# Optimization experiments

Hardware: AMD Instinct MI355X
Metric: run time of the kernel (lower is better)

Reference implementation:

```python
import jax, jax.numpy as jnp
import numpy as np

N_NODES = 65536
N_EDGES = 524288
IN_CH = 128
FHC = 256      # first_hc = max(hidden, in)
HID = 256
NCLS = 3
NODES_PER_GRAPH = 32


def setup_inputs() -> dict:
    key = jax.random.key(0)
    ks = jax.random.split(key, 16)
    s = 1.0 / np.sqrt(FHC)
    inp = {
        "x": jax.random.normal(ks[0], (N_NODES, IN_CH), dtype=jnp.float32),
        "edge_index": jax.random.randint(ks[1], (2, N_EDGES), 0, N_NODES, dtype=jnp.int64),
        "edge_attr": jax.random.uniform(ks[2], (N_EDGES,), dtype=jnp.float32),
        # GatedGraphConv params: per-layer matmul weight + GRUCell
        "gg_w": jax.random.uniform(ks[3], (2, FHC, FHC), minval=-s, maxval=s, dtype=jnp.float32),
        "w_ih": jax.random.uniform(ks[4], (3 * FHC, FHC), minval=-s, maxval=s, dtype=jnp.float32),
        "w_hh": jax.random.uniform(ks[5], (3 * FHC, FHC), minval=-s, maxval=s, dtype=jnp.float32),
        "b_ih": jax.random.uniform(ks[6], (3 * FHC,), minval=-s, maxval=s, dtype=jnp.float32),
        "b_hh": jax.random.uniform(ks[7], (3 * FHC,), minval=-s, maxval=s, dtype=jnp.float32),
        # Conv1d(FHC, 1, kernel_size=1)
        "cnn_w": jax.random.uniform(ks[8], (1, FHC, 1), minval=-s, maxval=s, dtype=jnp.float32),
        "cnn_b": jax.random.uniform(ks[9], (1,), minval=-s, maxval=s, dtype=jnp.float32),
        # Linear(32, HID), Linear(HID, NCLS)
        "lin1_w": jax.random.uniform(ks[10], (HID, NODES_PER_GRAPH), minval=-0.17, maxval=0.17, dtype=jnp.float32),
        "lin1_b": jax.random.uniform(ks[11], (HID,), minval=-0.17, maxval=0.17, dtype=jnp.float32),
        "lin2_w": jax.random.uniform(ks[12], (NCLS, HID), minval=-s, maxval=s, dtype=jnp.float32),
        "lin2_b": jax.random.uniform(ks[13], (NCLS,), minval=-s, maxval=s, dtype=jnp.float32),
    }
    return inp


def _gated_graph_conv(x, src, dst, edge_w, gg_w, w_ih, w_hh, b_ih, b_hh):
    # PyG GatedGraphConv: pad input to out_channels, then num_layers iterations.
    n = x.shape[0]
    h = jnp.pad(x, ((0, 0), (0, FHC - x.shape[1])))  # [N, FHC]
    for i in range(2):
        m = h @ gg_w[i]                                   # [N, FHC]
        msgs = m[src] * edge_w[:, None]                   # gather per edge [E, FHC]
        agg = jax.ops.segment_sum(msgs, dst, num_segments=n)  # scatter-add [N, FHC]
        # GRUCell(input=agg, hidden=h), torch gate order: r, z, n
        gi = agg @ w_ih.T + b_ih
        gh = h @ w_hh.T + b_hh
        ir, iz, ig = jnp.split(gi, 3, axis=1)
        hr, hz, hg = jnp.split(gh, 3, axis=1)
        r = jax.nn.sigmoid(ir + hr)
        z = jax.nn.sigmoid(iz + hz)
        g = jnp.tanh(ig + r * hg)
        h = (1.0 - z) * g + z * h
    return h


def reference(x, edge_index, edge_attr, gg_w, w_ih, w_hh, b_ih, b_hh,
              cnn_w, cnn_b, lin1_w, lin1_b, lin2_w, lin2_b):
    src, dst = edge_index[0], edge_index[1]
    h = _gated_graph_conv(x, src, dst, edge_attr, gg_w, w_ih, w_hh, b_ih, b_hh)
    h = jax.nn.relu(h)  # dropout is identity in eval mode
    bs = h.shape[0] // NODES_PER_GRAPH
    h = h.reshape(bs, NODES_PER_GRAPH, FHC)          # (bs e) f -> bs e f
    # Conv1d(FHC,1,k=1) over layout (bs, f, e): y[b,e] = sum_f w[0,f,0]*h[b,e,f] + b
    y = jnp.einsum('bef,f->be', h, cnn_w[:, :, 0].reshape(FHC)) + cnn_b[0]
    y = jax.nn.relu(y)                               # [bs, 32]
    y = y @ lin1_w.T + lin1_b
    y = jax.nn.relu(y)
    y = y @ lin2_w.T + lin2_b
    return jax.nn.softmax(y, axis=-1)
```

## Files before the change

kernel.cpp:

```cpp
#include <hip/hip_runtime.h>
#include <math.h>

#define N_NODES 65536
#define N_EDGES 524288
#define IN_CH 128
#define FHC 256
#define NCLS 3
#define NPG 32
#define NGRAPH (N_NODES / NPG)

typedef __attribute__((ext_vector_type(8))) short bfrag;
typedef __attribute__((ext_vector_type(4))) float facc;

__device__ inline float sigmoidf_(float x) { return 1.0f / (1.0f + expf(-x)); }

__device__ __forceinline__ float fast_sigmoid(float x) {
    return __builtin_amdgcn_rcpf(1.0f + __expf(-x));
}
__device__ __forceinline__ float fast_tanh(float x) {
    return 1.0f - 2.0f * __builtin_amdgcn_rcpf(__expf(2.0f * x) + 1.0f);
}

__device__ inline short f2bf(float f) {
    union { float f; unsigned u; } v; v.f = f;
    unsigned r = v.u + 0x7fffu + ((v.u >> 16) & 1u);
    return (short)(r >> 16);
}
__device__ inline float bf2f(short s) {
    union { unsigned u; float f; } v; v.u = ((unsigned)(unsigned short)s) << 16;
    return v.f;
}

__device__ __forceinline__ void gld16(const short* g, short* l) {
    __builtin_amdgcn_global_load_lds(
        (const __attribute__((address_space(1))) void*)g,
        (__attribute__((address_space(3))) void*)l, 16, 0, 0);
}

__global__ void convert_kernel(const float* __restrict__ gg_w, const float* __restrict__ wih,
                               const float* __restrict__ whh, short* __restrict__ ggT,
                               short* __restrict__ wih16, short* __restrict__ whh16) {
    int t = blockIdx.x * 256 + threadIdx.x;
    if (t < 2 * FHC * FHC) {
        int i = t >> 16, r = t & 65535, n = r >> 8, k = r & 255;
        ggT[t] = f2bf(gg_w[i * FHC * FHC + k * FHC + n]);
    } else if (t < 2 * FHC * FHC + 3 * FHC * FHC) {
        int u = t - 2 * FHC * FHC;
        wih16[u] = f2bf(wih[u]);
    } else {
        int u = t - 5 * FHC * FHC;
        whh16[u] = f2bf(whh[u]);
    }
}

__global__ void pad16_kernel(const float* __restrict__ x, short* __restrict__ h) {
    int idx = blockIdx.x * 256 + threadIdx.x;
    int c4 = idx & 63, n = idx >> 6;
    short4 v = {0, 0, 0, 0};
    if (c4 < 32) {
        float4 xv = reinterpret_cast<const float4*>(x)[n * 32 + c4];
        v.x = f2bf(xv.x); v.y = f2bf(xv.y); v.z = f2bf(xv.z); v.w = f2bf(xv.w);
    }
    reinterpret_cast<short4*>(h)[idx] = v;
}

__global__ void hist_kernel(const int* __restrict__ ei, int* __restrict__ deg) {
    int e = blockIdx.x * 256 + threadIdx.x;
    atomicAdd(&deg[ei[N_EDGES + e]], 1);
}

__global__ void scan_reduce_kernel(const int* __restrict__ deg, int* __restrict__ bsum) {
    __shared__ int s[256];
    int t = threadIdx.x;
    s[t] = deg[blockIdx.x * 256 + t];
    __syncthreads();
    for (int off = 128; off > 0; off >>= 1) {
        if (t < off) s[t] += s[t + off];
        __syncthreads();
    }
    if (t == 0) bsum[blockIdx.x] = s[0];
}

__global__ void scan_bsum_kernel(const int* __restrict__ bsum, int* __restrict__ boff) {
    __shared__ int s[256];
    int t = threadIdx.x;
    int v = bsum[t];
    s[t] = v;
    __syncthreads();
    for (int off = 1; off < 256; off <<= 1) {
        int u = (t >= off) ? s[t - off] : 0;
        __syncthreads();
        s[t] += u;
        __syncthreads();
    }
    boff[t] = s[t] - v;
}

__global__ void scan_write_kernel(const int* __restrict__ deg, const int* __restrict__ boff,
                                  int* __restrict__ rowptr, int* __restrict__ cur) {
    __shared__ int s[256];
    int t = threadIdx.x, gid = blockIdx.x * 256 + t;
    int v = deg[gid];
    s[t] = v;
    __syncthreads();
    for (int off = 1; off < 256; off <<= 1) {
        int u = (t >= off) ? s[t - off] : 0;
        __syncthreads();
        s[t] += u;
        __syncthreads();
    }
    int excl = boff[blockIdx.x] + s[t] - v;
    rowptr[gid] = excl;
    cur[gid] = excl;
    if (gid == N_NODES - 1) rowptr[N_NODES] = excl + v;
}

__global__ void fill_kernel(const int* __restrict__ ei, const float* __restrict__ ea,
                            int* __restrict__ cur, int2* __restrict__ csr) {
    int e = blockIdx.x * 256 + threadIdx.x;
    int dst = ei[N_EDGES + e];
    int pos = atomicAdd(&cur[dst], 1);
    csr[pos] = make_int2(ei[e], __float_as_int(ea[e]));
}

__global__ __launch_bounds__(256) void gather_kernel(const short* __restrict__ m,
                                                     const int* __restrict__ rowptr,
                                                     const int2* __restrict__ csr,
                                                     short* __restrict__ agg16) {
    int node = blockIdx.x * 4 + (threadIdx.x >> 6);
    int lane = threadIdx.x & 63;
    int beg = rowptr[node], end = rowptr[node + 1];
    const short4* m4 = reinterpret_cast<const short4*>(m);
    float a0 = 0.f, a1 = 0.f, a2 = 0.f, a3 = 0.f;
#define GSTEP(E)                                            \
    {                                                       \
        float w = __int_as_float((E).y);                    \
        short4 v = m4[(size_t)(E).x * 64 + lane];           \
        a0 += bf2f(v.x) * w;                                \
        a1 += bf2f(v.y) * w;                                \
        a2 += bf2f(v.z) * w;                                \
        a3 += bf2f(v.w) * w;                                \
    }
    int j = beg;
    for (; j + 8 <= end; j += 8) {
        int2 e0 = csr[j + 0], e1 = csr[j + 1], e2 = csr[j + 2], e3 = csr[j + 3];
        int2 e4 = csr[j + 4], e5 = csr[j + 5], e6 = csr[j + 6], e7 = csr[j + 7];
        GSTEP(e0) GSTEP(e1) GSTEP(e2) GSTEP(e3)
        GSTEP(e4) GSTEP(e5) GSTEP(e6) GSTEP(e7)
    }
    for (; j + 2 <= end; j += 2) {
        int2 e0 = csr[j + 0], e1 = csr[j + 1];
        GSTEP(e0) GSTEP(e1)
    }
    if (j < end) {
        int2 e0 = csr[j];
        GSTEP(e0)
    }
#undef GSTEP
    short4 o;
    o.x = f2bf(a0); o.y = f2bf(a1); o.z = f2bf(a2); o.w = f2bf(a3);
    reinterpret_cast<short4*>(agg16)[(size_t)node * 64 + lane] = o;
}

__global__ __launch_bounds__(256, 2) void mgemm_kernel(const short* __restrict__ A,
                                                       const short* __restrict__ W,
                                                       short* __restrict__ C) {
    __shared__ __align__(16) short As[128 * 32];
    __shared__ __align__(16) short Ws[128 * 32];
    int tid = threadIdx.x;
    int lane = tid & 63, wv = tid >> 6, fr = lane & 15, fc = lane >> 4;
    int m0 = blockIdx.x * 128, n0 = blockIdx.y * 128;
    int srow = lane >> 2;
    int scol = (lane & 3) ^ ((lane >> 3) & 3);
    const short* gsrc[4];
    short* ldst[4];
#pragma unroll
    for (int i = 0; i < 4; ++i) {
        int ch = wv * 4 + i;
        if (ch < 8) {
            ldst[i] = &As[ch * 512];
            gsrc[i] = A + (size_t)(m0 + ch * 16 + srow) * FHC + scol * 8;
        } else {
            ldst[i] = &Ws[(ch - 8) * 512];
            gsrc[i] = W + (size_t)(n0 + (ch - 8) * 16 + srow) * FHC + scol * 8;
        }
    }
    int fcs = fc ^ ((fr >> 1) & 3);
    facc acc[2][8] = {};
    for (int k0 = 0; k0 < FHC; k0 += 32) {
#pragma unroll
        for (int i = 0; i < 4; ++i) gld16(gsrc[i] + k0, ldst[i]);
        __syncthreads();
        int ar = (wv * 32 + fr) * 32 + fcs * 8;
        bfrag a0 = *reinterpret_cast<bfrag*>(&As[ar]);
        bfrag a1 = *reinterpret_cast<bfrag*>(&As[ar + 16 * 32]);
#pragma unroll
        for (int cf = 0; cf < 8; ++cf) {
            bfrag b = *reinterpret_cast<bfrag*>(&Ws[(cf * 16 + fr) * 32 + fcs * 8]);
            acc[0][cf] = __builtin_amdgcn_mfma_f32_16x16x32_bf16(a0, b, acc[0][cf], 0, 0, 0);
            acc[1][cf] = __builtin_amdgcn_mfma_f32_16x16x32_bf16(a1, b, acc[1][cf], 0, 0, 0);
        }
        __syncthreads();
    }
#pragma unroll
    for (int s = 0; s < 2; ++s)
#pragma unroll
        for (int cf = 0; cf < 8; ++cf)
#pragma unroll
            for (int r = 0; r < 4; ++r) {
                int node = m0 + wv * 32 + s * 16 + fc * 4 + r;
                int c = n0 + cf * 16 + fr;
                C[(size_t)node * FHC + c] = f2bf(acc[s][cf][r]);
            }
}

__global__ __launch_bounds__(256, 2) void gru_mfma_kernel(
    const short* __restrict__ agg16, const short* __restrict__ hin, short* __restrict__ hout,
    const short* __restrict__ wih16, const short* __restrict__ whh16,
    const float* __restrict__ bih, const float* __restrict__ bhh) {
    __shared__ __align__(16) short lds[2 * 16 * 512];
    int tid = threadIdx.x;
    int lane = tid & 63, wv = tid >> 6, fr = lane & 15, fc = lane >> 4;
    int c = blockIdx.y * 64 + wv * 16 + fr;

    bfrag wreg[6][8];
    {
        size_t roff = (size_t)c * FHC + fc * 8;
#pragma unroll
        for (int ks = 0; ks < 8; ++ks) {
            wreg[0][ks] = *reinterpret_cast<const bfrag*>(wih16 + roff + ks * 32);
            wreg[1][ks] = *reinterpret_cast<const bfrag*>(wih16 + (size_t)256 * FHC + roff + ks * 32);
            wreg[2][ks] = *reinterpret_cast<const bfrag*>(wih16 + (size_t)512 * FHC + roff + ks * 32);
            wreg[3][ks] = *reinterpret_cast<const bfrag*>(whh16 + roff + ks * 32);
            wreg[4][ks] = *reinterpret_cast<const bfrag*>(whh16 + (size_t)256 * FHC + roff + ks * 32);
            wreg[5][ks] = *reinterpret_cast<const bfrag*>(whh16 + (size_t)512 * FHC + roff + ks * 32);
        }
    }
    float br = bih[c] + bhh[c];
    float bz = bih[c + 256] + bhh[c + 256];
    float big = bih[c + 512], bhg = bhh[c + 512];

    int srow = lane >> 2;
    int scol = (lane & 3) ^ ((lane >> 3) & 3);
    const short* gb[4];
    int ldsoff[4];
#pragma unroll
    for (int i = 0; i < 4; ++i) {
        int ch = wv * 4 + i;
        int mat = ch >> 3, ks = ch & 7;
        const short* src = mat ? hin : agg16;
        gb[i] = src + (size_t)srow * FHC + ks * 32 + scol * 8;
        ldsoff[i] = ch * 512;
    }
    int fcs = fc ^ ((fr >> 1) & 3);
    int lo = (fr * 4 + fcs) * 8;
    const int NT = 32;
    int tile0 = blockIdx.x * NT;

    int hbase = (8 + (c >> 5)) * 512 + (c & 7);
    int hg = (c >> 3) & 3;

    auto STAGE = [&](int t, int bufsel) {
        size_t noff = (size_t)(tile0 + t) * 16 * FHC;
        short* dst = &lds[bufsel * 8192];
#pragma unroll
        for (int i = 0; i < 4; ++i) gld16(gb[i] + noff, dst + ldsoff[i]);
    };

    STAGE(0, 0);
    for (int t = 0; t < NT; ++t) {
        int cur = t & 1;
        if (t + 1 < NT) {
            STAGE(t + 1, cur ^ 1);
            asm volatile("s_waitcnt vmcnt(8)" ::: "memory");
        } else {
            asm volatile("s_waitcnt vmcnt(0)" ::: "memory");
        }
        __builtin_amdgcn_sched_barrier(0);
        __builtin_amdgcn_s_barrier();
        const short* B = &lds[cur * 8192];
        facc aR = {}, aZ = {}, aG = {}, aH = {};
#pragma unroll
        for (int ks = 0; ks < 8; ++ks) {
            bfrag ag = *reinterpret_cast<const bfrag*>(B + ks * 512 + lo);
            bfrag hh = *reinterpret_cast<const bfrag*>(B + (8 + ks) * 512 + lo);
            aR = __builtin_amdgcn_mfma_f32_16x16x32_bf16(ag, wreg[0][ks], aR, 0, 0, 0);
            aR = __builtin_amdgcn_mfma_f32_16x16x32_bf16(hh, wreg[3][ks], aR, 0, 0, 0);
            aZ = __builtin_amdgcn_mfma_f32_16x16x32_bf16(ag, wreg[1][ks], aZ, 0, 0, 0);
            aZ = __builtin_amdgcn_mfma_f32_16x16x32_bf16(hh, wreg[4][ks], aZ, 0, 0, 0);
            aG = __builtin_amdgcn_mfma_f32_16x16x32_bf16(ag, wreg[2][ks], aG, 0, 0, 0);
            aH = __builtin_amdgcn_mfma_f32_16x16x32_bf16(hh, wreg[5][ks], aH, 0, 0, 0);
        }
        int node0 = (tile0 + t) * 16;
#pragma unroll
        for (int r = 0; r < 4; ++r) {
            int row = fc * 4 + r;
            float hold = bf2f(B[hbase + (row * 4 + (hg ^ ((row >> 1) & 3))) * 8]);
            float rg = fast_sigmoid(aR[r] + br);
            float z = fast_sigmoid(aZ[r] + bz);
            float g = fast_tanh(aG[r] + big + rg * (aH[r] + bhg));
            hout[(size_t)(node0 + row) * FHC + c] = f2bf(g + z * (hold - g));
        }
        __builtin_amdgcn_s_barrier();
    }
}

__global__ void cnn_kernel(const short* __restrict__ h, const float* __restrict__ w,
                           const float* __restrict__ b, float* __restrict__ y1) {
    int node = blockIdx.x * 4 + (threadIdx.x >> 6);
    int lane = threadIdx.x & 63;
    short4 hv = reinterpret_cast<const short4*>(h)[(size_t)node * 64 + lane];
    float4 wv = reinterpret_cast<const float4*>(w)[lane];
    float p = fmaxf(bf2f(hv.x), 0.f) * wv.x + fmaxf(bf2f(hv.y), 0.f) * wv.y +
              fmaxf(bf2f(hv.z), 0.f) * wv.z + fmaxf(bf2f(hv.w), 0.f) * wv.w;
#pragma unroll
    for (int off = 32; off > 0; off >>= 1) p += __shfl_down(p, off, 64);
    if (lane == 0) y1[node] = fmaxf(p + b[0], 0.f);
}

__global__ __launch_bounds__(256) void head_kernel(
    const float* __restrict__ y1, const float* __restrict__ l1w,
    const float* __restrict__ l1b, const float* __restrict__ l2w,
    const float* __restrict__ l2b, float* __restrict__ out) {
    __shared__ float ys[32];
    __shared__ float zs[256];
    __shared__ float os[3];
    int b = blockIdx.x, tid = threadIdx.x;
    if (tid < 32) ys[tid] = y1[b * 32 + tid];
    __syncthreads();
    float acc = l1b[tid];
#pragma unroll
    for (int k = 0; k < 32; ++k) acc += ys[k] * l1w[tid * 32 + k];
    zs[tid] = fmaxf(acc, 0.f);
    __syncthreads();
    int wave = tid >> 6, lane = tid & 63;
    if (wave < 3) {
        float p = 0.f;
#pragma unroll
        for (int j = 0; j < 4; ++j) p += zs[lane + j * 64] * l2w[wave * 256 + lane + j * 64];
#pragma unroll
        for (int off = 32; off > 0; off >>= 1) p += __shfl_down(p, off, 64);
        if (lane == 0) os[wave] = p + l2b[wave];
    }
    __syncthreads();
    if (tid == 0) {
        float mx = fmaxf(os[0], fmaxf(os[1], os[2]));
        float e0 = expf(os[0] - mx), e1 = expf(os[1] - mx), e2 = expf(os[2] - mx);
        float s = e0 + e1 + e2;
        out[b * 3 + 0] = e0 / s;
        out[b * 3 + 1] = e1 / s;
        out[b * 3 + 2] = e2 / s;
    }
}

extern "C" void kernel_launch(void* const* d_in, const int* in_sizes, int n_in,
                              void* d_out, int out_size, void* d_ws, size_t ws_size,
                              hipStream_t stream) {
    const float* x = (const float*)d_in[0];
    const int* ei = (const int*)d_in[1];
    const float* ea = (const float*)d_in[2];
    const float* gg_w = (const float*)d_in[3];
    const float* w_ih = (const float*)d_in[4];
    const float* w_hh = (const float*)d_in[5];
    const float* b_ih = (const float*)d_in[6];
    const float* b_hh = (const float*)d_in[7];
    const float* cnn_w = (const float*)d_in[8];
    const float* cnn_b = (const float*)d_in[9];
    const float* l1w = (const float*)d_in[10];
    const float* l1b = (const float*)d_in[11];
    const float* l2w = (const float*)d_in[12];
    const float* l2b = (const float*)d_in[13];
    float* out = (float*)d_out;

    const size_t nodeE = (size_t)N_NODES * FHC;
    char* p = (char*)d_ws;
    short* hA = (short*)p;      p += nodeE * 2;
    short* hB = (short*)p;      p += nodeE * 2;
    short* m16 = (short*)p;     p += nodeE * 2;
    short* agg16 = (short*)p;   p += nodeE * 2;
    short* ggT = (short*)p;     p += (size_t)2 * FHC * FHC * 2;
    short* wih16 = (short*)p;   p += (size_t)3 * FHC * FHC * 2;
    short* whh16 = (short*)p;   p += (size_t)3 * FHC * FHC * 2;
    float* y1 = (float*)p;      p += (size_t)N_NODES * 4;
    int* deg = (int*)p;         p += (size_t)N_NODES * 4;
    int* rowptr = (int*)p;      p += (size_t)(N_NODES + 4) * 4;
    int* cur = (int*)p;         p += (size_t)N_NODES * 4;
    int* bsum = (int*)p;        p += 256 * 4;
    int* boff = (int*)p;        p += 256 * 4;
    int2* csr = (int2*)p;       p += (size_t)N_EDGES * 8;

    dim3 grid_gemm(N_NODES / 128, FHC / 128);
    dim3 grid_gru(128, 4);

    convert_kernel<<<8 * FHC * FHC / 256, 256, 0, stream>>>(gg_w, w_ih, w_hh, ggT, wih16, whh16);
    pad16_kernel<<<N_NODES * 64 / 256, 256, 0, stream>>>(x, hA);

    hipMemsetAsync(deg, 0, (size_t)N_NODES * 4, stream);
    hist_kernel<<<N_EDGES / 256, 256, 0, stream>>>(ei, deg);
    scan_reduce_kernel<<<N_NODES / 256, 256, 0, stream>>>(deg, bsum);
    scan_bsum_kernel<<<1, 256, 0, stream>>>(bsum, boff);
    scan_write_kernel<<<N_NODES / 256, 256, 0, stream>>>(deg, boff, rowptr, cur);
    fill_kernel<<<N_EDGES / 256, 256, 0, stream>>>(ei, ea, cur, csr);

    mgemm_kernel<<<grid_gemm, 256, 0, stream>>>(hA, ggT, m16);
    gather_kernel<<<N_NODES / 4, 256, 0, stream>>>(m16, rowptr, csr, agg16);
    gru_mfma_kernel<<<grid_gru, 256, 0, stream>>>(agg16, hA, hB, wih16, whh16, b_ih, b_hh);

    mgemm_kernel<<<grid_gemm, 256, 0, stream>>>(hB, ggT + FHC * FHC, m16);
    gather_kernel<<<N_NODES / 4, 256, 0, stream>>>(m16, rowptr, csr, agg16);
    gru_mfma_kernel<<<grid_gru, 256, 0, stream>>>(agg16, hB, hA, wih16, whh16, b_ih, b_hh);

    cnn_kernel<<<N_NODES / 4, 256, 0, stream>>>(hA, cnn_w, cnn_b, y1);
    head_kernel<<<NGRAPH, 256, 0, stream>>>(y1, l1w, l1b, l2w, l2b, out);
}
```

Measured before the change: 316.4 us.

## Triple-buffer LDS staging in mgemm and GRU kernels with prefetch distance two

Both MFMA kernels now rotate through three LDS buffers and prefetch two tiles ahead, using explicit vmcnt waits and a single barrier per iteration in place of the previous double-buffer or synchronous loads. The aim is to hide global-to-LDS load latency behind MFMA work and to drop the trailing barrier. MFMA sections are also wrapped in s_setprio to favour issuing matrix instructions. In exchange, LDS use grows, and the hand-counted vmcnt values must match the exact number of outstanding loads and stores.

```diff
diff --git a/kernel.cpp b/kernel.cpp
--- a/kernel.cpp
+++ b/kernel.cpp
@@ -165,42 +165,56 @@
 __global__ __launch_bounds__(256, 2) void mgemm_kernel(const short* __restrict__ A,
                                                        const short* __restrict__ W,
                                                        short* __restrict__ C) {
-    __shared__ __align__(16) short As[128 * 32];
-    __shared__ __align__(16) short Ws[128 * 32];
+    __shared__ __align__(16) short lds[3 * 16 * 512];
     int tid = threadIdx.x;
     int lane = tid & 63, wv = tid >> 6, fr = lane & 15, fc = lane >> 4;
     int m0 = blockIdx.x * 128, n0 = blockIdx.y * 128;
     int srow = lane >> 2;
     int scol = (lane & 3) ^ ((lane >> 3) & 3);
     const short* gsrc[4];
-    short* ldst[4];
+    int ldsoff[4];
 #pragma unroll
     for (int i = 0; i < 4; ++i) {
         int ch = wv * 4 + i;
         if (ch < 8) {
-            ldst[i] = &As[ch * 512];
+            ldsoff[i] = ch * 512;
             gsrc[i] = A + (size_t)(m0 + ch * 16 + srow) * FHC + scol * 8;
         } else {
-            ldst[i] = &Ws[(ch - 8) * 512];
+            ldsoff[i] = 4096 + (ch - 8) * 512;
             gsrc[i] = W + (size_t)(n0 + (ch - 8) * 16 + srow) * FHC + scol * 8;
         }
     }
     int fcs = fc ^ ((fr >> 1) & 3);
+
+    auto STAGE = [&](int ks, int bufsel) {
+        short* dst = &lds[bufsel * 8192];
+#pragma unroll
+        for (int i = 0; i < 4; ++i) gld16(gsrc[i] + ks * 32, dst + ldsoff[i]);
+    };
+
     facc acc[2][8] = {};
-    for (int k0 = 0; k0 < FHC; k0 += 32) {
-#pragma unroll
-        for (int i = 0; i < 4; ++i) gld16(gsrc[i] + k0, ldst[i]);
-        __syncthreads();
+    STAGE(0, 0);
+    STAGE(1, 1);
+    for (int ks = 0; ks < 8; ++ks) {
+        if (ks < 7) { asm volatile("s_waitcnt vmcnt(4)" ::: "memory"); }
+        else        { asm volatile("s_waitcnt vmcnt(0)" ::: "memory"); }
+        __builtin_amdgcn_sched_barrier(0);
+        __builtin_amdgcn_s_barrier();
+        __builtin_amdgcn_sched_barrier(0);
+        if (ks + 2 < 8) STAGE(ks + 2, (ks + 2) % 3);
+        __builtin_amdgcn_sched_barrier(0);
+        const short* B = &lds[(ks % 3) * 8192];
         int ar = (wv * 32 + fr) * 32 + fcs * 8;
-        bfrag a0 = *reinterpret_cast<bfrag*>(&As[ar]);
-        bfrag a1 = *reinterpret_cast<bfrag*>(&As[ar + 16 * 32]);
+        bfrag a0 = *reinterpret_cast<const bfrag*>(B + ar);
+        bfrag a1 = *reinterpret_cast<const bfrag*>(B + ar + 16 * 32);
+        __builtin_amdgcn_s_setprio(1);
 #pragma unroll
         for (int cf = 0; cf < 8; ++cf) {
-            bfrag b = *reinterpret_cast<bfrag*>(&Ws[(cf * 16 + fr) * 32 + fcs * 8]);
+            bfrag b = *reinterpret_cast<const bfrag*>(B + 4096 + (cf * 16 + fr) * 32 + fcs * 8);
             acc[0][cf] = __builtin_amdgcn_mfma_f32_16x16x32_bf16(a0, b, acc[0][cf], 0, 0, 0);
             acc[1][cf] = __builtin_amdgcn_mfma_f32_16x16x32_bf16(a1, b, acc[1][cf], 0, 0, 0);
         }
-        __syncthreads();
+        __builtin_amdgcn_s_setprio(0);
     }
 #pragma unroll
     for (int s = 0; s < 2; ++s)
@@ -218,7 +232,7 @@
     const short* __restrict__ agg16, const short* __restrict__ hin, short* __restrict__ hout,
     const short* __restrict__ wih16, const short* __restrict__ whh16,
     const float* __restrict__ bih, const float* __restrict__ bhh) {
-    __shared__ __align__(16) short lds[2 * 16 * 512];
+    __shared__ __align__(16) short lds[3 * 16 * 512];
     int tid = threadIdx.x;
     int lane = tid & 63, wv = tid >> 6, fr = lane & 15, fc = lane >> 4;
     int c = blockIdx.y * 64 + wv * 16 + fr;
@@ -268,18 +282,19 @@
     };
 
     STAGE(0, 0);
+    STAGE(1, 1);
     for (int t = 0; t < NT; ++t) {
-        int cur = t & 1;
-        if (t + 1 < NT) {
-            STAGE(t + 1, cur ^ 1);
-            asm volatile("s_waitcnt vmcnt(8)" ::: "memory");
-        } else {
-            asm volatile("s_waitcnt vmcnt(0)" ::: "memory");
-        }
+        if (t == 0)                   { asm volatile("s_waitcnt vmcnt(4)" ::: "memory"); }
+        else if (t == 1 || t == NT-1) { asm volatile("s_waitcnt vmcnt(8)" ::: "memory"); }
+        else                          { asm volatile("s_waitcnt vmcnt(12)" ::: "memory"); }
         __builtin_amdgcn_sched_barrier(0);
         __builtin_amdgcn_s_barrier();
-        const short* B = &lds[cur * 8192];
+        __builtin_amdgcn_sched_barrier(0);
+        if (t + 2 < NT) STAGE(t + 2, (t + 2) % 3);
+        __builtin_amdgcn_sched_barrier(0);
+        const short* B = &lds[(t % 3) * 8192];
         facc aR = {}, aZ = {}, aG = {}, aH = {};
+        __builtin_amdgcn_s_setprio(1);
 #pragma unroll
         for (int ks = 0; ks < 8; ++ks) {
             bfrag ag = *reinterpret_cast<const bfrag*>(B + ks * 512 + lo);
@@ -291,6 +306,7 @@
             aG = __builtin_amdgcn_mfma_f32_16x16x32_bf16(ag, wreg[2][ks], aG, 0, 0, 0);
             aH = __builtin_amdgcn_mfma_f32_16x16x32_bf16(hh, wreg[5][ks], aH, 0, 0, 0);
         }
+        __builtin_amdgcn_s_setprio(0);
         int node0 = (tile0 + t) * 16;
 #pragma unroll
         for (int r = 0; r < 4; ++r) {
@@ -301,7 +317,6 @@
             float g = fast_tanh(aG[r] + big + rg * (aH[r] + bhg));
             hout[(size_t)(node0 + row) * FHC + c] = f2bf(g + z * (hold - g));
         }
-        __builtin_amdgcn_s_barrier();
     }
 }
 
```

New measurement: 319.7 us. Within noise of the previous version (+1.1%).
